# Kernel tuning notes

Hardware: AMD Instinct MI355X
Metric: run time of the kernel (lower is better)

## Reference

```python
import jax, jax.numpy as jnp
import numpy as np
from jax import lax

SEQ_LEN = 8192
TAGS = 2048

def setup_inputs() -> dict:
    key = jax.random.key(0)
    k1, k2, k3, k4, k5 = jax.random.split(key, 5)
    feats = jax.random.normal(k1, (SEQ_LEN, TAGS), dtype=jnp.float32)
    tags = jax.random.randint(k2, (SEQ_LEN,), 0, TAGS, dtype=jnp.int32)
    # nn.Parameter(torch.rand(...)) -> uniform [0,1)
    transitions = jax.random.uniform(k3, (TAGS, TAGS), dtype=jnp.float32)
    transitions_start = jax.random.uniform(k4, (TAGS,), dtype=jnp.float32)
    transitions_stop = jax.random.uniform(k5, (TAGS,), dtype=jnp.float32)
    return {
        "feats": feats,
        "transitions": transitions,
        "transitions_start": transitions_start,
        "transitions_stop": transitions_stop,
        "tags": tags,
    }

def reference(feats, transitions, transitions_start, transitions_stop, tags):
    # Linear-chain CRF negative log-likelihood.
    # transitions[next, prev] = score of transitioning prev -> next.
    L = feats.shape[0]

    # ---- forward (partition) score via log-sum-exp recurrence ----
    fv0 = transitions_start + feats[0]  # [T]

    def step(fv, feat):
        # new[j] = logsumexp_i(fv[i] + transitions[j, i]) + feat[j]
        nfv = jax.nn.logsumexp(fv[None, :] + transitions, axis=1) + feat
        return nfv, None

    fv, _ = lax.scan(step, fv0, feats[1:])
    forward_score = jax.nn.logsumexp(fv + transitions_stop)

    # ---- gold path score ----
    gold = (
        transitions_start[tags[0]]
        + feats[0, tags[0]]
        + jnp.sum(transitions[tags[1:], tags[:-1]])
        + jnp.sum(feats[jnp.arange(1, L), tags[1:]])
        + transitions_stop[tags[-1]]
    )

    return forward_score - gold
```

## Files before the change

kernel.cpp:

```cpp
#include <hip/hip_runtime.h>

#define SEQ  8192
#define NT   2048
#define NBLK 256
#define NTHR 512
#define LOG2E 1.4426950408889634f
#define LN2   0.6931471805599453f

#define STORE_AG(p, v) __hip_atomic_store((p), (v), __ATOMIC_RELAXED, __HIP_MEMORY_SCOPE_AGENT)

typedef unsigned int u32x4 __attribute__((ext_vector_type(4)));

__device__ __forceinline__ u32x4 poll_load16(const unsigned int* p) {
    u32x4 r;
    asm volatile("global_load_dwordx4 %0, %1, off sc0 sc1\n\t"
                 "s_waitcnt vmcnt(0)"
                 : "=v"(r) : "v"(p) : "memory");
    return r;
}

__device__ __align__(16) unsigned int g_z[2][NT];
__device__ float g_gold;

__device__ __forceinline__ unsigned int f32_to_bf16(float f) {
    unsigned int u = __float_as_uint(f);
    return (u + 0x7FFFu + ((u >> 16) & 1u)) >> 16;
}

__global__ void crf_init(const float* __restrict__ feats,
                         const float* __restrict__ tstart) {
    int i = blockIdx.x * blockDim.x + threadIdx.x;
    if (i < NT) {
        float z0 = __builtin_exp2f((tstart[i] + feats[i]) * LOG2E);
        g_z[0][i] = f32_to_bf16(z0);
        g_z[1][i] = 0xFFFF0000u;
    }
}

__global__ void crf_gold(const float* __restrict__ feats,
                         const float* __restrict__ trans,
                         const float* __restrict__ tstart,
                         const float* __restrict__ tstop,
                         const int*   __restrict__ tags) {
    __shared__ float part[16];
    int tid = threadIdx.x;
    float acc = 0.f;
    for (int t = 1 + tid; t < SEQ; t += 1024) {
        int cur = tags[t], prev = tags[t - 1];
        acc += trans[(size_t)cur * NT + prev] + feats[(size_t)t * NT + cur];
    }
    #pragma unroll
    for (int m = 1; m < 64; m <<= 1) acc += __shfl_xor(acc, m, 64);
    if ((tid & 63) == 0) part[tid >> 6] = acc;
    __syncthreads();
    if (tid == 0) {
        float S = 0.f;
        #pragma unroll
        for (int w = 0; w < 16; ++w) S += part[w];
        int t0 = tags[0], tl = tags[SEQ - 1];
        g_gold = S + tstart[t0] + feats[t0] + tstop[tl];
    }
}

__global__ void __launch_bounds__(NTHR)
crf_main(const float* __restrict__ feats, const float* __restrict__ trans,
         const float* __restrict__ tstop, float* __restrict__ out) {
    const int b   = blockIdx.x;
    const int tid = threadIdx.x;
    const int wid = tid >> 6;
    const int l   = tid & 63;
    const int j   = b * 8 + wid;

    __shared__ float w_lds[2][NT];
    __shared__ float s_scale[2];
    __shared__ unsigned int pk[8];
    __shared__ float red[8];

    float E[32];
    {
        const float* trow = trans + (size_t)j * NT;
        #pragma unroll
        for (int k = 0; k < 32; ++k)
            E[k] = __builtin_exp2f(trow[l + (k << 6)] * LOG2E);
    }

    float fexp = __builtin_exp2f(feats[(size_t)NT + j] * LOG2E);
    int esum = 0;

    for (int t = 1; t < SEQ; ++t) {
        const int par = (t - 1) & 1;
        const unsigned int need = (unsigned int)(t - 1);
        const unsigned int* buf = g_z[par] + 4 * tid;

        u32x4 v;
        do { v = poll_load16(buf); }
        while ((v.x >> 16) != need || (v.y >> 16) != need ||
               (v.z >> 16) != need || (v.w >> 16) != need);

        w_lds[par][4 * tid + 0] = __uint_as_float(v.x << 16);
        w_lds[par][4 * tid + 1] = __uint_as_float(v.y << 16);
        w_lds[par][4 * tid + 2] = __uint_as_float(v.z << 16);
        w_lds[par][4 * tid + 3] = __uint_as_float(v.w << 16);

        if (tid == 0) {
            int e = (int)((v.x >> 7) & 0xFFu) - 127;
            s_scale[par] = __uint_as_float((unsigned int)(127 - e) << 23);
            esum += e;
        }
        float fexpnext = (t + 1 < SEQ)
            ? __builtin_exp2f(feats[(size_t)(t + 1) * NT + j] * LOG2E) : 0.f;
        __syncthreads();

        float acc = 0.f;
        #pragma unroll
        for (int k = 0; k < 32; ++k)
            acc = fmaf(E[k], w_lds[par][l + (k << 6)], acc);
        #pragma unroll
        for (int m = 1; m < 64; m <<= 1) acc += __shfl_xor(acc, m, 64);

        if (l == 0) {
            float znew = acc * s_scale[par] * fexp;
            pk[wid] = ((unsigned int)t << 16) | f32_to_bf16(znew);
        }
        fexp = fexpnext;
        __syncthreads();

        if (tid < 8) STORE_AG(&g_z[t & 1][b * 8 + tid], pk[tid]);
    }

    if (b == 0) {
        const unsigned int need = SEQ - 1;
        const unsigned int* buf = g_z[(SEQ - 1) & 1] + 4 * tid;
        u32x4 v;
        do { v = poll_load16(buf); }
        while ((v.x >> 16) != need || (v.y >> 16) != need ||
               (v.z >> 16) != need || (v.w >> 16) != need);

        float acc =
            __uint_as_float(v.x << 16) * __builtin_exp2f(tstop[4 * tid + 0] * LOG2E) +
            __uint_as_float(v.y << 16) * __builtin_exp2f(tstop[4 * tid + 1] * LOG2E) +
            __uint_as_float(v.z << 16) * __builtin_exp2f(tstop[4 * tid + 2] * LOG2E) +
            __uint_as_float(v.w << 16) * __builtin_exp2f(tstop[4 * tid + 3] * LOG2E);
        #pragma unroll
        for (int m = 1; m < 64; m <<= 1) acc += __shfl_xor(acc, m, 64);
        if (l == 0) red[wid] = acc;
        __syncthreads();
        if (tid == 0) {
            float S = 0.f;
            #pragma unroll
            for (int w = 0; w < 8; ++w) S += red[w];
            float fwd = (__builtin_log2f(S) + (float)esum) * LN2;
            out[0] = fwd - g_gold;
        }
    }
}

extern "C" void kernel_launch(void* const* d_in, const int* in_sizes, int n_in,
                              void* d_out, int out_size, void* d_ws, size_t ws_size,
                              hipStream_t stream) {
    const float* feats  = (const float*)d_in[0];
    const float* trans  = (const float*)d_in[1];
    const float* tstart = (const float*)d_in[2];
    const float* tstop  = (const float*)d_in[3];
    const int*   tags   = (const int*)d_in[4];
    float* out = (float*)d_out;

    hipLaunchKernelGGL(crf_init, dim3(2), dim3(1024), 0, stream, feats, tstart);
    hipLaunchKernelGGL(crf_gold, dim3(1), dim3(1024), 0, stream,
                       feats, trans, tstart, tstop, tags);
    hipLaunchKernelGGL(crf_main, dim3(NBLK), dim3(NTHR), 0, stream,
                       feats, trans, tstop, out);
}
```

Baseline: 21.28 ms.

## Compute partial dot products from polled registers, drop LDS staging and second barrier

Each thread now holds a 4-column by 8-row slice of exp(transitions) and multiplies it directly against the four bf16 values it polled, so the previous-step vector is no longer staged through LDS. Per-wave partial sums for the 8 output tags go through a small shared buffer and are reduced by wave 0, which also computes the scale and writes the packed results to global memory. This removes one of the two block barriers and the LDS write/read of the full state vector on the serial critical path. In exchange, every wave now runs 8 interleaved 6-step shuffle reductions per step, and wave 0 does extra serial work after the remaining barrier.

```diff
diff --git a/kernel.cpp b/kernel.cpp
--- a/kernel.cpp
+++ b/kernel.cpp
@@ -67,72 +67,89 @@
          const float* __restrict__ tstop, float* __restrict__ out) {
     const int b   = blockIdx.x;
     const int tid = threadIdx.x;
-    const int wid = tid >> 6;
+    const int wv  = tid >> 6;
     const int l   = tid & 63;
-    const int j   = b * 8 + wid;
 
-    __shared__ float w_lds[2][NT];
-    __shared__ float s_scale[2];
-    __shared__ unsigned int pk[8];
-    __shared__ float red[8];
+    __shared__ float part[2][64];
 
-    float E[32];
+    float E[8][4];
     {
-        const float* trow = trans + (size_t)j * NT;
+        const float* tb = trans + (size_t)(b * 8) * NT + 4 * tid;
         #pragma unroll
-        for (int k = 0; k < 32; ++k)
-            E[k] = __builtin_exp2f(trow[l + (k << 6)] * LOG2E);
+        for (int r = 0; r < 8; ++r) {
+            #pragma unroll
+            for (int q = 0; q < 4; ++q)
+                E[r][q] = __builtin_exp2f(tb[(size_t)r * NT + q] * LOG2E);
+        }
     }
 
-    float fexp = __builtin_exp2f(feats[(size_t)NT + j] * LOG2E);
+    float fexp = 0.f;
+    if (wv == 0 && l < 8)
+        fexp = __builtin_exp2f(feats[(size_t)NT + b * 8 + l] * LOG2E);
     int esum = 0;
 
     for (int t = 1; t < SEQ; ++t) {
         const int par = (t - 1) & 1;
         const unsigned int need = (unsigned int)(t - 1);
-        const unsigned int* buf = g_z[par] + 4 * tid;
 
         u32x4 v;
-        do { v = poll_load16(buf); }
+        do { v = poll_load16(g_z[par] + 4 * tid); }
         while ((v.x >> 16) != need || (v.y >> 16) != need ||
                (v.z >> 16) != need || (v.w >> 16) != need);
 
-        w_lds[par][4 * tid + 0] = __uint_as_float(v.x << 16);
-        w_lds[par][4 * tid + 1] = __uint_as_float(v.y << 16);
-        w_lds[par][4 * tid + 2] = __uint_as_float(v.z << 16);
-        w_lds[par][4 * tid + 3] = __uint_as_float(v.w << 16);
+        const float w0 = __uint_as_float(v.x << 16);
+        const float w1 = __uint_as_float(v.y << 16);
+        const float w2 = __uint_as_float(v.z << 16);
+        const float w3 = __uint_as_float(v.w << 16);
 
-        if (tid == 0) {
-            int e = (int)((v.x >> 7) & 0xFFu) - 127;
-            s_scale[par] = __uint_as_float((unsigned int)(127 - e) << 23);
-            esum += e;
+        float p[8];
+        #pragma unroll
+        for (int r = 0; r < 8; ++r) {
+            float a = E[r][0] * w0;
+            a = fmaf(E[r][1], w1, a);
+            a = fmaf(E[r][2], w2, a);
+            a = fmaf(E[r][3], w3, a);
+            p[r] = a;
         }
-        float fexpnext = (t + 1 < SEQ)
-            ? __builtin_exp2f(feats[(size_t)(t + 1) * NT + j] * LOG2E) : 0.f;
+        #pragma unroll
+        for (int m = 1; m < 64; m <<= 1) {
+            #pragma unroll
+            for (int r = 0; r < 8; ++r) p[r] += __shfl_xor(p[r], m, 64);
+        }
+        if (l == 0) {
+            #pragma unroll
+            for (int r = 0; r < 8; ++r) part[par][wv * 8 + r] = p[r];
+        }
+
+        float scale = 0.f, fexpnext = 0.f;
+        if (wv == 0) {
+            unsigned int w0bits = __shfl(v.x, 0, 64);
+            int e = (int)((w0bits >> 7) & 0xFFu) - 127;
+            scale = __uint_as_float((unsigned int)(127 - e) << 23);
+            if (tid == 0) esum += e;
+            if (l < 8 && t + 1 < SEQ)
+                fexpnext = __builtin_exp2f(feats[(size_t)(t + 1) * NT + b * 8 + l] * LOG2E);
+        }
         __syncthreads();
 
-        float acc = 0.f;
-        #pragma unroll
-        for (int k = 0; k < 32; ++k)
-            acc = fmaf(E[k], w_lds[par][l + (k << 6)], acc);
-        #pragma unroll
-        for (int m = 1; m < 64; m <<= 1) acc += __shfl_xor(acc, m, 64);
-
-        if (l == 0) {
-            float znew = acc * s_scale[par] * fexp;
-            pk[wid] = ((unsigned int)t << 16) | f32_to_bf16(znew);
+        if (wv == 0) {
+            float val = part[par][l];
+            #pragma unroll
+            for (int m = 8; m < 64; m <<= 1) val += __shfl_xor(val, m, 64);
+            if (l < 8) {
+                float znew = val * scale * fexp;
+                STORE_AG(&g_z[t & 1][b * 8 + l],
+                         ((unsigned int)t << 16) | f32_to_bf16(znew));
+            }
+            fexp = fexpnext;
         }
-        fexp = fexpnext;
-        __syncthreads();
-
-        if (tid < 8) STORE_AG(&g_z[t & 1][b * 8 + tid], pk[tid]);
     }
 
     if (b == 0) {
+        __shared__ float red[8];
         const unsigned int need = SEQ - 1;
-        const unsigned int* buf = g_z[(SEQ - 1) & 1] + 4 * tid;
         u32x4 v;
-        do { v = poll_load16(buf); }
+        do { v = poll_load16(g_z[(SEQ - 1) & 1] + 4 * tid); }
         while ((v.x >> 16) != need || (v.y >> 16) != need ||
                (v.z >> 16) != need || (v.w >> 16) != need);
 
@@ -143,7 +160,7 @@
             __uint_as_float(v.w << 16) * __builtin_exp2f(tstop[4 * tid + 3] * LOG2E);
         #pragma unroll
         for (int m = 1; m < 64; m <<= 1) acc += __shfl_xor(acc, m, 64);
-        if (l == 0) red[wid] = acc;
+        if (l == 0) red[wv] = acc;
         __syncthreads();
         if (tid == 0) {
             float S = 0.f;
```

New measurement: 27.53 ms. +29.4%, slower.
